# Kernel optimization log

Hardware: AMD Instinct MI355X
Metric: run time of the kernel (lower is better)

The kernel has to match this reference:

```python
import jax, jax.numpy as jnp
import numpy as np
import math

S = 30.0
M = 0.5
COS_M = math.cos(M)
SIN_M = math.sin(M)
TH = math.cos(math.pi - M)
MM = math.sin(math.pi - M) * M
B, D, C = 512, 512, 100000


def setup_inputs() -> dict:
    key = jax.random.key(0)
    k1, k2, k3 = jax.random.split(key, 3)
    inp = jax.random.normal(k1, (B, D), dtype=jnp.float32)
    weight = jax.random.normal(k2, (C, D), dtype=jnp.float32) * (1.0 / math.sqrt(D))
    label = jax.random.randint(k3, (B,), 0, C, dtype=jnp.int64)
    return {"input": inp, "label": label, "weight": weight}


def _l2norm(x, axis=-1, eps=1e-12):
    # matches F.normalize: x / max(||x||, eps)
    n = jnp.sqrt(jnp.sum(x * x, axis=axis, keepdims=True))
    return x / jnp.maximum(n, eps)


def reference(input, label, weight):
    # cosine: [B, C]
    cosine = jnp.clip(_l2norm(input) @ _l2norm(weight).T, -1.0, 1.0)
    sine = jnp.sqrt(jnp.clip(1.0 - cosine * cosine, 1e-9, 1.0))
    phi = cosine * COS_M - sine * SIN_M
    phi = jnp.where(cosine > TH, phi, cosine - MM)  # easy_margin=False branch
    one_hot = (label[:, None] == jnp.arange(cosine.shape[1])[None, :])
    out = jnp.where(one_hot, phi, cosine) * S
    return out
```

## Files before the change

kernel.cpp:

```cpp
#include <hip/hip_runtime.h>
#include <hip/hip_bf16.h>

#define ARC_S    30.0f
#define ARC_COSM 0.8775825618903728f
#define ARC_SINM 0.4794255386042030f
#define ARC_TH  -0.8775825618903728f
#define ARC_MM   0.2397127693021015f

#define B_ROWS 512
#define D_DIM  512
#define C_CLS  100000
#define C_PAD  100096

typedef float  floatx4 __attribute__((ext_vector_type(4)));
typedef __bf16 bf16x8  __attribute__((ext_vector_type(8)));

__global__ __launch_bounds__(256) void normalize_rows_512(
    const float* __restrict__ src, __bf16* __restrict__ dst, int valid_rows)
{
    const int lane = threadIdx.x & 63;
    const int wave = threadIdx.x >> 6;
    const long long row = (long long)blockIdx.x * 4 + wave;

    __bf16* drow = dst + row * D_DIM;

    if (row >= valid_rows) {
        bf16x8 z;
        #pragma unroll
        for (int i = 0; i < 8; i++) z[i] = (__bf16)0.0f;
        *(bf16x8*)(drow + lane * 8) = z;
        return;
    }

    const float4* rp = (const float4*)(src + row * D_DIM);
    float4 p0 = rp[lane * 2];
    float4 p1 = rp[lane * 2 + 1];

    float ss = p0.x*p0.x + p0.y*p0.y + p0.z*p0.z + p0.w*p0.w
             + p1.x*p1.x + p1.y*p1.y + p1.z*p1.z + p1.w*p1.w;
    #pragma unroll
    for (int m = 32; m >= 1; m >>= 1) ss += __shfl_xor(ss, m, 64);

    const float scale = 1.0f / fmaxf(sqrtf(ss), 1e-12f);

    bf16x8 v;
    v[0] = (__bf16)(p0.x * scale);
    v[1] = (__bf16)(p0.y * scale);
    v[2] = (__bf16)(p0.z * scale);
    v[3] = (__bf16)(p0.w * scale);
    v[4] = (__bf16)(p1.x * scale);
    v[5] = (__bf16)(p1.y * scale);
    v[6] = (__bf16)(p1.z * scale);
    v[7] = (__bf16)(p1.w * scale);
    *(bf16x8*)(drow + lane * 8) = v;
}

#define BM 256
#define BN 128
#define BK 64
#define N_TILES 782
#define GRID_B  1568

__device__ inline void async_load_16B(__bf16* lds, const __bf16* gmem)
{
    __builtin_amdgcn_global_load_lds(
        (const __attribute__((address_space(1))) void*)gmem,
        (__attribute__((address_space(3))) void*)lds,
        16, 0, 0);
}

__global__ __launch_bounds__(512, 4) void gemm_arcface(
    const __bf16* __restrict__ A,
    const __bf16* __restrict__ W,
    const int*    __restrict__ label,
    float*        __restrict__ out)
{
    const int b  = blockIdx.x;
    const int nt = (b & 7) + 8 * (b >> 4);
    const int mt = (b >> 3) & 1;
    if (nt >= N_TILES) return;

    __shared__ __bf16 As[BM * BK];
    __shared__ __bf16 Bs[BN * BK];
    __shared__ int    sLab[BM];

    const int tid = threadIdx.x;
    const int m0  = mt * BM;
    const int n0  = nt * BN;

    if (tid < BM) sLab[tid] = label[m0 + tid];

    const int lane = tid & 63;
    const int wave = tid >> 6;
    const int wr   = wave >> 1;
    const int wc   = wave & 1;

    floatx4 acc[4][4];
    #pragma unroll
    for (int i = 0; i < 4; i++)
        #pragma unroll
        for (int j = 0; j < 4; j++)
            acc[i][j] = (floatx4)(0.0f);

    const int frow = lane & 15;
    const int fch  = lane >> 4;

    for (int k0 = 0; k0 < D_DIM; k0 += BK) {
        if (k0) __syncthreads();
        #pragma unroll
        for (int r = 0; r < 4; r++) {
            const int i   = r * 512 + tid;
            const int row = i >> 3;
            const int kc  = i & 7;
            const int kcs = kc ^ (row & 7);
            async_load_16B(As + i * 8, A + (long long)(m0 + row) * D_DIM + k0 + kcs * 8);
        }
        #pragma unroll
        for (int r = 0; r < 2; r++) {
            const int i   = r * 512 + tid;
            const int row = i >> 3;
            const int kc  = i & 7;
            const int kcs = kc ^ (row & 7);
            async_load_16B(Bs + i * 8, W + (long long)(n0 + row) * D_DIM + k0 + kcs * 8);
        }
        __syncthreads();

        #pragma unroll
        for (int ks = 0; ks < 2; ks++) {
            const int ch = ks * 4 + fch;
            bf16x8 a[4], bb[4];
            #pragma unroll
            for (int i = 0; i < 4; i++) {
                const int ar = wr * 64 + i * 16 + frow;
                a[i] = *(const bf16x8*)(As + ar * BK + ((ch ^ (ar & 7)) << 3));
            }
            #pragma unroll
            for (int j = 0; j < 4; j++) {
                const int br = wc * 64 + j * 16 + frow;
                bb[j] = *(const bf16x8*)(Bs + br * BK + ((ch ^ (br & 7)) << 3));
            }
            #pragma unroll
            for (int i = 0; i < 4; i++)
                #pragma unroll
                for (int j = 0; j < 4; j++)
                    acc[i][j] = __builtin_amdgcn_mfma_f32_16x16x32_bf16(
                        a[i], bb[j], acc[i][j], 0, 0, 0);
        }
    }

    const int mrow = (lane >> 4) * 4;
    const int ncol = lane & 15;

    #pragma unroll
    for (int i = 0; i < 4; i++) {
        #pragma unroll
        for (int r = 0; r < 4; r++) {
            const int ml  = wr * 64 + i * 16 + mrow + r;
            const int m   = m0 + ml;
            const int lab = sLab[ml];
            float* orow = out + (long long)m * C_CLS;
            #pragma unroll
            for (int j = 0; j < 4; j++) {
                const int cls = n0 + wc * 64 + j * 16 + ncol;
                if (cls < C_CLS) {
                    float c = fminf(fmaxf(acc[i][j][r], -1.0f), 1.0f);
                    float t = fminf(fmaxf(1.0f - c * c, 1e-9f), 1.0f);
                    float s = sqrtf(t);
                    float phi = c * ARC_COSM - s * ARC_SINM;
                    phi = (c > ARC_TH) ? phi : (c - ARC_MM);
                    float o = ((lab == cls) ? phi : c) * ARC_S;
                    orow[cls] = o;
                }
            }
        }
    }
}

extern "C" void kernel_launch(void* const* d_in, const int* in_sizes, int n_in,
                              void* d_out, int out_size, void* d_ws, size_t ws_size,
                              hipStream_t stream)
{
    const float* inp    = (const float*)d_in[0];
    const int*   label  = (const int*)d_in[1];
    const float* weight = (const float*)d_in[2];
    float*       out    = (float*)d_out;

    __bf16* A = (__bf16*)d_ws;
    __bf16* W = A + (size_t)B_ROWS * D_DIM;

    normalize_rows_512<<<B_ROWS / 4, 256, 0, stream>>>(inp, A, B_ROWS);
    normalize_rows_512<<<C_PAD / 4, 256, 0, stream>>>(weight, W, C_CLS);
    gemm_arcface<<<GRID_B, 512, 0, stream>>>(A, W, label, out);
}
```

Measured before the change: 437.5 us.

## Double-buffer LDS tiles with BK=32 and prefetch the next K-step during MFMA

The K tile shrinks from 64 to 32 and LDS is split into two buffers per operand. The async global-to-LDS loads for step t+1 are issued before the MFMAs for step t, so load latency can overlap compute, and only one barrier is needed per step. Per-lane LDS fragment offsets are precomputed with a new XOR swizzle matched to the 4-chunk rows. MFMA issue is wrapped in s_setprio. The cost is twice as many K iterations and barriers, and the output-store-heavy epilogue is left unchanged, so it may still dominate.

```diff
diff --git a/kernel.cpp b/kernel.cpp
--- a/kernel.cpp
+++ b/kernel.cpp
@@ -57,7 +57,8 @@
 
 #define BM 256
 #define BN 128
-#define BK 64
+#define BK 32
+#define KSTEPS  (D_DIM / BK)
 #define N_TILES 782
 #define GRID_B  1568
 
@@ -80,8 +81,8 @@
     const int mt = (b >> 3) & 1;
     if (nt >= N_TILES) return;
 
-    __shared__ __bf16 As[BM * BK];
-    __shared__ __bf16 Bs[BN * BK];
+    __shared__ __bf16 As[2][BM * BK];
+    __shared__ __bf16 Bs[2][BN * BK];
     __shared__ int    sLab[BM];
 
     const int tid = threadIdx.x;
@@ -94,6 +95,24 @@
     const int wave = tid >> 6;
     const int wr   = wave >> 1;
     const int wc   = wave & 1;
+    const int frow = lane & 15;
+    const int fch  = lane >> 4;
+
+    const int srow = tid >> 2;
+    const int skc  = (tid & 3) ^ ((tid >> 3) & 3);
+
+    const __bf16* gA0 = A + (long long)(m0 + srow) * D_DIM + skc * 8;
+    const __bf16* gA1 = gA0 + (long long)128 * D_DIM;
+    const __bf16* gB0 = W + (long long)(n0 + srow) * D_DIM + skc * 8;
+
+    int aoff[4], boff[4];
+    #pragma unroll
+    for (int i = 0; i < 4; i++) {
+        const int ar = wr * 64 + i * 16 + frow;
+        aoff[i] = ar * BK + ((fch ^ ((ar >> 1) & 3)) << 3);
+        const int br = wc * 64 + i * 16 + frow;
+        boff[i] = br * BK + ((fch ^ ((br >> 1) & 3)) << 3);
+    }
 
     floatx4 acc[4][4];
     #pragma unroll
@@ -102,50 +121,37 @@
         for (int j = 0; j < 4; j++)
             acc[i][j] = (floatx4)(0.0f);
 
-    const int frow = lane & 15;
-    const int fch  = lane >> 4;
-
-    for (int k0 = 0; k0 < D_DIM; k0 += BK) {
-        if (k0) __syncthreads();
-        #pragma unroll
-        for (int r = 0; r < 4; r++) {
-            const int i   = r * 512 + tid;
-            const int row = i >> 3;
-            const int kc  = i & 7;
-            const int kcs = kc ^ (row & 7);
-            async_load_16B(As + i * 8, A + (long long)(m0 + row) * D_DIM + k0 + kcs * 8);
+    async_load_16B(&As[0][tid * 8],         gA0);
+    async_load_16B(&As[0][(tid + 512) * 8], gA1);
+    async_load_16B(&Bs[0][tid * 8],         gB0);
+    __syncthreads();
+
+    #pragma unroll 2
+    for (int t = 0; t < KSTEPS; ++t) {
+        const int cur = t & 1;
+        if (t + 1 < KSTEPS) {
+            const int ko = (t + 1) * BK;
+            async_load_16B(&As[cur ^ 1][tid * 8],         gA0 + ko);
+            async_load_16B(&As[cur ^ 1][(tid + 512) * 8], gA1 + ko);
+            async_load_16B(&Bs[cur ^ 1][tid * 8],         gB0 + ko);
         }
-        #pragma unroll
-        for (int r = 0; r < 2; r++) {
-            const int i   = r * 512 + tid;
-            const int row = i >> 3;
-            const int kc  = i & 7;
-            const int kcs = kc ^ (row & 7);
-            async_load_16B(Bs + i * 8, W + (long long)(n0 + row) * D_DIM + k0 + kcs * 8);
-        }
-        __syncthreads();
-
-        #pragma unroll
-        for (int ks = 0; ks < 2; ks++) {
-            const int ch = ks * 4 + fch;
-            bf16x8 a[4], bb[4];
+
+        bf16x8 a[4], bb[4];
+        #pragma unroll
+        for (int i = 0; i < 4; i++) a[i]  = *(const bf16x8*)(&As[cur][aoff[i]]);
+        #pragma unroll
+        for (int j = 0; j < 4; j++) bb[j] = *(const bf16x8*)(&Bs[cur][boff[j]]);
+
+        __builtin_amdgcn_s_setprio(1);
+        #pragma unroll
+        for (int i = 0; i < 4; i++)
             #pragma unroll
-            for (int i = 0; i < 4; i++) {
-                const int ar = wr * 64 + i * 16 + frow;
-                a[i] = *(const bf16x8*)(As + ar * BK + ((ch ^ (ar & 7)) << 3));
-            }
-            #pragma unroll
-            for (int j = 0; j < 4; j++) {
-                const int br = wc * 64 + j * 16 + frow;
-                bb[j] = *(const bf16x8*)(Bs + br * BK + ((ch ^ (br & 7)) << 3));
-            }
-            #pragma unroll
-            for (int i = 0; i < 4; i++)
-                #pragma unroll
-                for (int j = 0; j < 4; j++)
-                    acc[i][j] = __builtin_amdgcn_mfma_f32_16x16x32_bf16(
-                        a[i], bb[j], acc[i][j], 0, 0, 0);
-        }
+            for (int j = 0; j < 4; j++)
+                acc[i][j] = __builtin_amdgcn_mfma_f32_16x16x32_bf16(
+                    a[i], bb[j], acc[i][j], 0, 0, 0);
+        __builtin_amdgcn_s_setprio(0);
+
+        if (t + 1 < KSTEPS) __syncthreads();
     }
 
     const int mrow = (lane >> 4) * 4;
```

Result: no change. 443.8 us (+1.4%).
